# Performance work log

Measured on AMD Instinct MI355X. Metric: run time of the kernel, lower is better.

The kernel has to match this reference:

```python
import jax, jax.numpy as jnp
import numpy as np

B, D, H, O, E, K = 16384, 128, 512, 128, 8, 2
T = 1.0
EPS = float(np.finfo(float).eps)  # combine() zero-fill epsilon


def cv_squared(v):
    # torch .var() is unbiased (ddof=1)
    return jnp.var(v, ddof=1) / (jnp.mean(v) ** 2 + 1e-10)


def setup_inputs() -> dict:
    key = jax.random.key(0)
    k0, k1, k2, k3, k4, k5 = jax.random.split(key, 6)
    x = jax.random.normal(k0, (B, D), dtype=jnp.float32)
    w_gate = jax.random.normal(k1, (D, E), dtype=jnp.float32) * 0.02
    w1 = jax.random.normal(k2, (E, D, H), dtype=jnp.float32) * (1.0 / np.sqrt(D))
    b1 = jax.random.normal(k3, (E, H), dtype=jnp.float32) * 0.01
    w2 = jax.random.normal(k4, (E, H, O), dtype=jnp.float32) * (1.0 / np.sqrt(H))
    b2 = jax.random.normal(k5, (E, O), dtype=jnp.float32) * 0.01
    return {"x": x, "w_gate": w_gate, "w1": w1, "b1": b1, "w2": w2, "b2": b2}


def reference(x, w_gate, w1, b1, w2, b2):
    # ---- noisy top-k gating (eval mode: clean logits, no noise) ----
    logits = x @ w_gate                                   # [B, E]
    top_logits, top_idx = jax.lax.top_k(logits, K)        # [B, K]
    top_gates = jax.nn.softmax(top_logits / T, axis=-1)   # [B, K]
    gates = jnp.zeros_like(logits).at[jnp.arange(x.shape[0])[:, None], top_idx].set(top_gates)

    importance = gates.sum(0)                              # [E]
    load = (gates > 0).sum(0).astype(jnp.float32)          # [E]
    loss = cv_squared(importance) + cv_squared(load)

    # ---- experts (dense gate-weighted form of dispatch/combine) ----
    # output[b] = Sum_i gates[b,i] * expert_i(x[b]); zero gates contribute nothing,
    # identical math to SparseDispatcher's gather / per-expert MLP / scatter-add.
    h = jax.nn.relu(jnp.einsum('bd,edh->beh', x, w1) + b1[None])   # [B, E, H]
    y_e = jnp.einsum('beh,eho->beo', h, w2) + b2[None]             # [B, E, O]
    y = jnp.einsum('be,beo->bo', gates, y_e)                       # [B, O]
    # combine(): combined[combined == 0] = eps
    y = jnp.where(y == 0, jnp.asarray(EPS, y.dtype), y)
    return y, loss
```

## Files before the change

kernel.cpp:

```cpp
#include <hip/hip_runtime.h>
#include <hip/hip_bf16.h>
#include <math.h>

#define NB 16384
#define ND 128
#define NH 512
#define NO 128
#define NE 8
#define CPAD 32
#define NCH 16
#define EPSF 2.2204460492503131e-16f

using bf16x8 = __attribute__((ext_vector_type(8))) short;
using f32x16 = __attribute__((ext_vector_type(16))) float;
using uint2v = __attribute__((ext_vector_type(2))) unsigned;

#define WS_COUNTS 0u
#define WS_IMP    1024u
#define WS_TOKID  2048u
#define WS_TOKGG  526336u
#define WS_XBF    657408u
#define WS_W1F    4851712u
#define WS_W2F    5900288u
#define WS_YSTAGE 6948864u

__device__ __forceinline__ unsigned f2bf(float f){
  unsigned u = __float_as_uint(f);
  u += 0x7FFFu + ((u >> 16) & 1u);
  return u >> 16;
}
__device__ __forceinline__ unsigned cvtpk(float lo, float hi){
  unsigned r;
  asm("v_cvt_pk_bf16_f32 %0, %1, %2" : "=v"(r) : "v"(lo), "v"(hi));
  return r;
}
__device__ __forceinline__ void gld16(const void* g, void* l){
  __builtin_amdgcn_global_load_lds((const __attribute__((address_space(1))) void*)g,
                                   (__attribute__((address_space(3))) void*)l, 16, 0, 0);
}

__global__ __launch_bounds__(256) void prep_kernel(
    const float* __restrict__ x, const float* __restrict__ wg,
    const float* __restrict__ w1, const float* __restrict__ w2,
    unsigned short* __restrict__ xbf, unsigned short* __restrict__ w1f,
    unsigned short* __restrict__ w2f, int* __restrict__ counts,
    float* __restrict__ imp, int* __restrict__ tok_ids, float2* __restrict__ tok_gg){
  int bx = blockIdx.x, tid = threadIdx.x;
  if (bx >= 512){
    int u = (bx - 512)*256 + tid;
    int o = u & 127, hb = (u>>7)&3, c = (u>>9)&15, e = u>>13;
    int h0 = c*32 + (hb>>1)*16 + (hb&1)*8;
    const float* src = w2 + (size_t)e*NH*NO + (size_t)h0*NO + o;
    unsigned q[4];
    #pragma unroll
    for (int p = 0; p < 4; ++p)
      q[p] = f2bf(src[(2*p)*NO]) | (f2bf(src[(2*p+1)*NO]) << 16);
    *(uint4*)(w2f + (size_t)u*8) = make_uint4(q[0], q[1], q[2], q[3]);
    return;
  }
  if (bx >= 256){
    int u = (bx - 256)*256 + tid;
    int h32 = u & 31, db = (u>>5)&15, c = (u>>9)&15, e = u>>13;
    int d0 = (db>>1)*16 + (db&1)*8;
    int hg = c*32 + h32;
    const float* src = w1 + (size_t)e*ND*NH + (size_t)d0*NH + hg;
    unsigned q[4];
    #pragma unroll
    for (int p = 0; p < 4; ++p)
      q[p] = f2bf(src[(2*p)*NH]) | (f2bf(src[(2*p+1)*NH]) << 16);
    *(uint4*)(w1f + (size_t)u*8) = make_uint4(q[0], q[1], q[2], q[3]);
    return;
  }
  __shared__ int   lcnt[NE];
  __shared__ float limp[NE];
  __shared__ int   lbase[NE];
  if (tid < NE){ lcnt[tid] = 0; limp[tid] = 0.f; }
  __syncthreads();
  int tok  = bx*64 + (tid >> 2);
  int part = tid & 3;
  const float4* xr4 = (const float4*)(x + (size_t)tok*ND);
  double acc[NE];
  #pragma unroll
  for (int e = 0; e < NE; ++e) acc[e] = 0.0;
  #pragma unroll
  for (int j = 0; j < 8; ++j){
    int f4 = part + j*4;
    float4 v = xr4[f4];
    uint2 p;
    p.x = f2bf(v.x) | (f2bf(v.y) << 16);
    p.y = f2bf(v.z) | (f2bf(v.w) << 16);
    *(uint2*)(xbf + (size_t)tok*ND + f4*4) = p;
    const float4* wr = (const float4*)(wg + f4*32);
    float vm[4] = {v.x, v.y, v.z, v.w};
    #pragma unroll
    for (int m = 0; m < 4; ++m){
      float4 wa = wr[2*m], wb = wr[2*m+1];
      double d = (double)vm[m];
      acc[0] += d*(double)wa.x; acc[1] += d*(double)wa.y;
      acc[2] += d*(double)wa.z; acc[3] += d*(double)wa.w;
      acc[4] += d*(double)wb.x; acc[5] += d*(double)wb.y;
      acc[6] += d*(double)wb.z; acc[7] += d*(double)wb.w;
    }
  }
  #pragma unroll
  for (int e = 0; e < NE; ++e){
    acc[e] += __shfl_xor(acc[e], 1);
    acc[e] += __shfl_xor(acc[e], 2);
  }
  int i0 = 0, i1 = 0, s0 = 0, s1 = 0;
  float g0 = 0.f, g1 = 0.f;
  if (part == 0){
    double l0 = acc[0];
    #pragma unroll
    for (int e = 1; e < NE; ++e) if (acc[e] > l0){ l0 = acc[e]; i0 = e; }
    i1 = (i0 == 0) ? 1 : 0;
    double l1 = acc[i1];
    #pragma unroll
    for (int e = 0; e < NE; ++e) if (e != i0 && acc[e] > l1){ l1 = acc[e]; i1 = e; }
    float e1 = expf((float)(l1 - l0));
    g0 = 1.0f/(1.0f + e1);
    g1 = e1/(1.0f + e1);
    s0 = atomicAdd(&lcnt[i0], 1);
    s1 = atomicAdd(&lcnt[i1], 1);
    atomicAdd(&limp[i0], g0);
    atomicAdd(&limp[i1], g1);
    tok_gg[tok] = make_float2(g0, g1);
  }
  __syncthreads();
  if (tid < NE){
    lbase[tid] = atomicAdd(&counts[tid*CPAD], lcnt[tid]);
    atomicAdd(&imp[tid*CPAD], limp[tid]);
  }
  __syncthreads();
  if (part == 0){
    tok_ids[i0*NB + lbase[i0] + s0] = tok;
    tok_ids[i1*NB + lbase[i1] + s1] = tok | (1 << 30);
  }
}

__global__ __launch_bounds__(256) void expert_kernel(
    const unsigned short* __restrict__ xbf, const unsigned short* __restrict__ w1f,
    const unsigned short* __restrict__ w2f, const float* __restrict__ b1,
    const float* __restrict__ b2, const int* __restrict__ counts,
    const int* __restrict__ tok_ids, const float2* __restrict__ tok_gg,
    unsigned short* __restrict__ ystage){
  __shared__ char smem[32768];
  int b = blockIdx.x;
  int e = 0, base = 0, accb = 0, n_e = 0;
  #pragma unroll
  for (int ee = 0; ee < NE; ++ee){
    int ne = counts[ee*CPAD];
    int nbl = (ne + 127) >> 7;
    if (e == 0 && base == 0 && b < accb + nbl && n_e == 0){
      e = ee; base = (b - accb)*128; n_e = ne;
    }
    accb += nbl;
  }
  if (b >= accb) return;
  if (n_e == 0) return;
  int tid = threadIdx.x, wid = tid >> 6, lane = tid & 63, l31 = lane & 31, hi = lane >> 5;
  const int* tid_e = tok_ids + e*NB;
  char* w1buf = smem;
  char* w2buf = smem + 16384;
  const char* g1base = (const char*)w1f + ((size_t)e*NCH)*8192;
  const char* g2base = (const char*)w2f + ((size_t)e*NCH)*8192;

  int slot0 = base + wid*32 + l31;
  int raw0 = tid_e[slot0 < n_e ? slot0 : n_e-1];
  int tok0 = raw0 & 0x3FFFFFFF;
  bf16x8 xfrag[8];
  #pragma unroll
  for (int k = 0; k < 8; ++k)
    xfrag[k] = *(const bf16x8*)(xbf + (size_t)tok0*ND + (k*2 + hi)*8);

#define STAGE(c, bsel) do { \
    const char* _g1 = g1base + (size_t)(c)*8192 + wid*1024 + lane*16; \
    const char* _g2 = g2base + (size_t)(c)*8192 + wid*1024 + lane*16; \
    char* _l1 = w1buf + (bsel)*8192 + wid*1024; \
    char* _l2 = w2buf + (bsel)*8192 + wid*1024; \
    _Pragma("unroll") \
    for (int _s = 0; _s < 2; ++_s){ \
      gld16(_g1 + _s*4096, _l1 + _s*4096); \
      gld16(_g2 + _s*4096, _l2 + _s*4096); \
    } \
  } while(0)

  STAGE(0, 0);
  f32x16 yacc[4];
  #pragma unroll
  for (int ot = 0; ot < 4; ++ot)
    #pragma unroll
    for (int i = 0; i < 16; ++i) yacc[ot][i] = 0.f;
  __syncthreads();

  for (int c = 0; c < NCH; ++c){
    int bb = c & 1;
    if (c + 1 < NCH) STAGE(c + 1, bb ^ 1);
    f32x16 hacc;
    #pragma unroll
    for (int i = 0; i < 16; ++i) hacc[i] = 0.f;
    #pragma unroll
    for (int k = 0; k < 8; ++k){
      bf16x8 a = *(const bf16x8*)(w1buf + bb*8192 + (k*2 + hi)*512 + l31*16);
      hacc = __builtin_amdgcn_mfma_f32_32x32x16_bf16(a, xfrag[k], hacc, 0, 0, 0);
    }
    const float4* b1p = (const float4*)(b1 + e*NH + c*32 + hi*4);
    float dv[16];
    #pragma unroll
    for (int g = 0; g < 4; ++g){
      float4 bv = b1p[2*g];
      dv[4*g+0] = fmaxf(hacc[4*g+0] + bv.x, 0.f);
      dv[4*g+1] = fmaxf(hacc[4*g+1] + bv.y, 0.f);
      dv[4*g+2] = fmaxf(hacc[4*g+2] + bv.z, 0.f);
      dv[4*g+3] = fmaxf(hacc[4*g+3] + bv.w, 0.f);
    }
    unsigned A0 = cvtpk(dv[0], dv[1]),  A1 = cvtpk(dv[2], dv[3]);
    unsigned A2 = cvtpk(dv[4], dv[5]),  A3 = cvtpk(dv[6], dv[7]);
    unsigned A4 = cvtpk(dv[8], dv[9]),  A5 = cvtpk(dv[10], dv[11]);
    unsigned A6 = cvtpk(dv[12], dv[13]), A7 = cvtpk(dv[14], dv[15]);
    uint2v r0 = __builtin_amdgcn_permlane32_swap(A0, A2, false, false);
    uint2v r1 = __builtin_amdgcn_permlane32_swap(A1, A3, false, false);
    uint2v r2 = __builtin_amdgcn_permlane32_swap(A4, A6, false, false);
    uint2v r3 = __builtin_amdgcn_permlane32_swap(A5, A7, false, false);
    union { unsigned u[4]; bf16x8 v; } fa, fb;
    fa.u[0] = r0[0]; fa.u[1] = r1[0]; fa.u[2] = r0[1]; fa.u[3] = r1[1];
    fb.u[0] = r2[0]; fb.u[1] = r3[0]; fb.u[2] = r2[1]; fb.u[3] = r3[1];
    bf16x8 aht0 = fa.v, aht1 = fb.v;
    #pragma unroll
    for (int ot = 0; ot < 4; ++ot){
      bf16x8 bf0 = *(const bf16x8*)(w2buf + bb*8192 + (0*2 + hi)*2048 + (ot*32 + l31)*16);
      yacc[ot] = __builtin_amdgcn_mfma_f32_32x32x16_bf16(aht0, bf0, yacc[ot], 0, 0, 0);
      bf16x8 bf1 = *(const bf16x8*)(w2buf + bb*8192 + (1*2 + hi)*2048 + (ot*32 + l31)*16);
      yacc[ot] = __builtin_amdgcn_mfma_f32_32x32x16_bf16(aht1, bf1, yacc[ot], 0, 0, 0);
    }
    __syncthreads();
  }
#undef STAGE
  float b2v[4];
  #pragma unroll
  for (int ot = 0; ot < 4; ++ot) b2v[ot] = b2[e*NO + ot*32 + l31];
  #pragma unroll
  for (int r = 0; r < 16; ++r){
    int row = (r & 3) + 8*(r >> 2) + 4*hi;
    int slot = base + wid*32 + row;
    if (slot < n_e){
      int rw = tid_e[slot];
      int tk = rw & 0x3FFFFFFF, wh = (rw >> 30) & 1;
      float2 gg = tok_gg[tk];
      float g = wh ? gg.y : gg.x;
      unsigned short* dst = ystage + ((size_t)tk*2 + wh)*NO + l31;
      #pragma unroll
      for (int ot = 0; ot < 4; ++ot)
        dst[ot*32] = (unsigned short)f2bf((yacc[ot][r] + b2v[ot]) * g);
    }
  }
}

__global__ __launch_bounds__(256) void combine_kernel(
    const unsigned short* __restrict__ ystage, const int* __restrict__ counts,
    const float* __restrict__ imp, float* __restrict__ y){
  if (blockIdx.x == 0 && threadIdx.x == 0){
    double si = 0, sqi = 0, sl = 0, sql = 0;
    for (int e = 0; e < NE; ++e){
      double a = imp[e*CPAD];
      double b = (double)counts[e*CPAD];
      si += a; sqi += a*a; sl += b; sql += b*b;
    }
    double mi = si/8.0, vi = (sqi - 8.0*mi*mi)/7.0;
    double ml = sl/8.0, vl = (sql - 8.0*ml*ml)/7.0;
    y[NB*NO] = (float)(vi/(mi*mi + 1e-10) + vl/(ml*ml + 1e-10));
  }
  int idx = blockIdx.x*256 + threadIdx.x;
  int tk = idx >> 4, q = idx & 15;
  const unsigned short* r0 = ystage + (size_t)tk*256 + q*8;
  uint4 a = *(const uint4*)r0;
  uint4 bq = *(const uint4*)(r0 + 128);
  unsigned aw[4] = {a.x, a.y, a.z, a.w};
  unsigned bw[4] = {bq.x, bq.y, bq.z, bq.w};
  float4 o0, o1;
  float* op[8] = {&o0.x,&o0.y,&o0.z,&o0.w,&o1.x,&o1.y,&o1.z,&o1.w};
  #pragma unroll
  for (int i = 0; i < 4; ++i){
    float vlo = __uint_as_float(aw[i] << 16)        + __uint_as_float(bw[i] << 16);
    float vhi = __uint_as_float(aw[i] & 0xFFFF0000u) + __uint_as_float(bw[i] & 0xFFFF0000u);
    *op[2*i]   = (vlo == 0.f) ? EPSF : vlo;
    *op[2*i+1] = (vhi == 0.f) ? EPSF : vhi;
  }
  float* dst = y + (size_t)tk*128 + q*8;
  *(float4*)dst     = o0;
  *(float4*)(dst+4) = o1;
}

extern "C" void kernel_launch(void* const* d_in, const int* in_sizes, int n_in,
                              void* d_out, int out_size, void* d_ws, size_t ws_size,
                              hipStream_t stream){
  (void)in_sizes; (void)n_in; (void)out_size; (void)ws_size;
  const float* x  = (const float*)d_in[0];
  const float* wg = (const float*)d_in[1];
  const float* w1 = (const float*)d_in[2];
  const float* b1 = (const float*)d_in[3];
  const float* w2 = (const float*)d_in[4];
  const float* b2 = (const float*)d_in[5];
  float* out = (float*)d_out;
  char* ws = (char*)d_ws;
  int*            counts  = (int*)(ws + WS_COUNTS);
  float*          imp     = (float*)(ws + WS_IMP);
  int*            tok_ids = (int*)(ws + WS_TOKID);
  float2*         tok_gg  = (float2*)(ws + WS_TOKGG);
  unsigned short* xbf     = (unsigned short*)(ws + WS_XBF);
  unsigned short* w1f     = (unsigned short*)(ws + WS_W1F);
  unsigned short* w2f     = (unsigned short*)(ws + WS_W2F);
  unsigned short* ystage  = (unsigned short*)(ws + WS_YSTAGE);

  hipMemsetAsync(d_ws, 0, 2048, stream);
  prep_kernel<<<768, 256, 0, stream>>>(x, wg, w1, w2, xbf, w1f, w2f,
                                       counts, imp, tok_ids, tok_gg);
  expert_kernel<<<264, 256, 0, stream>>>(xbf, w1f, w2f, b1, b2,
                                         counts, tok_ids, tok_gg, ystage);
  combine_kernel<<<1024, 256, 0, stream>>>(ystage, counts, imp, out);
}
```

Before: 55.12 us.

## Fuse prep, expert and combine kernels into one persistent kernel with grid barriers

Merges the three launches into a single 256-block persistent kernel separated by software grid barriers. Per-block expert counts replace global atomics, and each block rebuilds the token-to-expert mapping itself with an LDS prefix scan. Expert tiles are looped over by the persistent blocks. This removes launch gaps and the atomic offset contention. It relies on all 256 blocks being co-resident for the spin barrier, and it adds per-tile scan and search overhead plus a redundant loop in the combine stage.

Result: slower. 197.3 us (+257.8%).

```diff
diff --git a/kernel.cpp b/kernel.cpp
--- a/kernel.cpp
+++ b/kernel.cpp
@@ -7,22 +7,31 @@
 #define NH 512
 #define NO 128
 #define NE 8
-#define CPAD 32
 #define NCH 16
+#define NBLK 256
 #define EPSF 2.2204460492503131e-16f
 
 using bf16x8 = __attribute__((ext_vector_type(8))) short;
 using f32x16 = __attribute__((ext_vector_type(16))) float;
 using uint2v = __attribute__((ext_vector_type(2))) unsigned;
 
-#define WS_COUNTS 0u
-#define WS_IMP    1024u
-#define WS_TOKID  2048u
-#define WS_TOKGG  526336u
-#define WS_XBF    657408u
-#define WS_W1F    4851712u
-#define WS_W2F    5900288u
-#define WS_YSTAGE 6948864u
+#define WS_BAR    0u
+#define WS_BLKCNT 1024u
+#define WS_BLKIMP 9216u
+#define WS_TOKID  17408u
+#define WS_TOKGG  541696u
+#define WS_XBF    672768u
+#define WS_W1F    4867072u
+#define WS_W2F    5915648u
+#define WS_YST    6964224u
+
+#define L_WB    0u
+#define L_CNT   32768u
+#define L_GP    40960u
+#define L_TOTL  41984u
+#define L_TBASE 42048u
+#define L_SLTOK 42112u
+#define L_A     42624u
 
 __device__ __forceinline__ unsigned f2bf(float f){
   unsigned u = __float_as_uint(f);
@@ -38,16 +47,43 @@
   __builtin_amdgcn_global_load_lds((const __attribute__((address_space(1))) void*)g,
                                    (__attribute__((address_space(3))) void*)l, 16, 0, 0);
 }
-
-__global__ __launch_bounds__(256) void prep_kernel(
+__device__ __forceinline__ void grid_barrier(int* bar, int target){
+  __syncthreads();
+  if (threadIdx.x == 0){
+    __threadfence();
+    __hip_atomic_fetch_add(bar, 1, __ATOMIC_RELEASE, __HIP_MEMORY_SCOPE_AGENT);
+    while (__hip_atomic_load(bar, __ATOMIC_ACQUIRE, __HIP_MEMORY_SCOPE_AGENT) < target)
+      __builtin_amdgcn_s_sleep(2);
+  }
+  __syncthreads();
+  __threadfence();
+}
+
+__global__ __launch_bounds__(256, 1) void moe_kernel(
     const float* __restrict__ x, const float* __restrict__ wg,
-    const float* __restrict__ w1, const float* __restrict__ w2,
+    const float* __restrict__ w1, const float* __restrict__ b1,
+    const float* __restrict__ w2, const float* __restrict__ b2,
+    int* __restrict__ bar, int* __restrict__ blk_cnt, float* __restrict__ blk_imp,
+    int* __restrict__ tok_ids, float2* __restrict__ tok_gg,
     unsigned short* __restrict__ xbf, unsigned short* __restrict__ w1f,
-    unsigned short* __restrict__ w2f, int* __restrict__ counts,
-    float* __restrict__ imp, int* __restrict__ tok_ids, float2* __restrict__ tok_gg){
-  int bx = blockIdx.x, tid = threadIdx.x;
-  if (bx >= 512){
-    int u = (bx - 512)*256 + tid;
+    unsigned short* __restrict__ w2f, unsigned short* __restrict__ ystage,
+    float* __restrict__ y){
+  __shared__ char L[43520];
+  int blk = blockIdx.x, tid = threadIdx.x;
+
+  {
+    int u = blk*256 + tid;
+    int h32 = u & 31, db = (u>>5)&15, c = (u>>9)&15, e = u>>13;
+    int d0 = (db>>1)*16 + (db&1)*8;
+    const float* src = w1 + (size_t)e*ND*NH + (size_t)d0*NH + c*32 + h32;
+    unsigned q[4];
+    #pragma unroll
+    for (int p = 0; p < 4; ++p)
+      q[p] = f2bf(src[(2*p)*NH]) | (f2bf(src[(2*p+1)*NH]) << 16);
+    *(uint4*)(w1f + (size_t)u*8) = make_uint4(q[0], q[1], q[2], q[3]);
+  }
+  {
+    int u = blk*256 + tid;
     int o = u & 127, hb = (u>>7)&3, c = (u>>9)&15, e = u>>13;
     int h0 = c*32 + (hb>>1)*16 + (hb&1)*8;
     const float* src = w2 + (size_t)e*NH*NO + (size_t)h0*NO + o;
@@ -56,122 +92,145 @@
     for (int p = 0; p < 4; ++p)
       q[p] = f2bf(src[(2*p)*NO]) | (f2bf(src[(2*p+1)*NO]) << 16);
     *(uint4*)(w2f + (size_t)u*8) = make_uint4(q[0], q[1], q[2], q[3]);
-    return;
-  }
-  if (bx >= 256){
-    int u = (bx - 256)*256 + tid;
-    int h32 = u & 31, db = (u>>5)&15, c = (u>>9)&15, e = u>>13;
-    int d0 = (db>>1)*16 + (db&1)*8;
-    int hg = c*32 + h32;
-    const float* src = w1 + (size_t)e*ND*NH + (size_t)d0*NH + hg;
-    unsigned q[4];
-    #pragma unroll
-    for (int p = 0; p < 4; ++p)
-      q[p] = f2bf(src[(2*p)*NH]) | (f2bf(src[(2*p+1)*NH]) << 16);
-    *(uint4*)(w1f + (size_t)u*8) = make_uint4(q[0], q[1], q[2], q[3]);
-    return;
-  }
-  __shared__ int   lcnt[NE];
-  __shared__ float limp[NE];
-  __shared__ int   lbase[NE];
-  if (tid < NE){ lcnt[tid] = 0; limp[tid] = 0.f; }
+  }
+  {
+    int*   lcnt = (int*)(L + L_A);
+    float* limp = (float*)(L + L_A + 32);
+    if (tid < NE){ lcnt[tid] = 0; limp[tid] = 0.f; }
+    __syncthreads();
+    int tok  = blk*64 + (tid >> 2);
+    int part = tid & 3;
+    const float4* xr4 = (const float4*)(x + (size_t)tok*ND);
+    double acc[NE];
+    #pragma unroll
+    for (int e = 0; e < NE; ++e) acc[e] = 0.0;
+    #pragma unroll
+    for (int j = 0; j < 8; ++j){
+      int f4 = part + j*4;
+      float4 v = xr4[f4];
+      uint2 p;
+      p.x = f2bf(v.x) | (f2bf(v.y) << 16);
+      p.y = f2bf(v.z) | (f2bf(v.w) << 16);
+      *(uint2*)(xbf + (size_t)tok*ND + f4*4) = p;
+      const float4* wr = (const float4*)(wg + f4*32);
+      float vm[4] = {v.x, v.y, v.z, v.w};
+      #pragma unroll
+      for (int m = 0; m < 4; ++m){
+        float4 wa = wr[2*m], wb = wr[2*m+1];
+        double d = (double)vm[m];
+        acc[0] += d*(double)wa.x; acc[1] += d*(double)wa.y;
+        acc[2] += d*(double)wa.z; acc[3] += d*(double)wa.w;
+        acc[4] += d*(double)wb.x; acc[5] += d*(double)wb.y;
+        acc[6] += d*(double)wb.z; acc[7] += d*(double)wb.w;
+      }
+    }
+    #pragma unroll
+    for (int e = 0; e < NE; ++e){
+      acc[e] += __shfl_xor(acc[e], 1);
+      acc[e] += __shfl_xor(acc[e], 2);
+    }
+    if (part == 0){
+      int i0 = 0;
+      double l0 = acc[0];
+      #pragma unroll
+      for (int e = 1; e < NE; ++e) if (acc[e] > l0){ l0 = acc[e]; i0 = e; }
+      int i1 = (i0 == 0) ? 1 : 0;
+      double l1 = acc[i1];
+      #pragma unroll
+      for (int e = 0; e < NE; ++e) if (e != i0 && acc[e] > l1){ l1 = acc[e]; i1 = e; }
+      float e1 = expf((float)(l1 - l0));
+      float g0 = 1.0f/(1.0f + e1);
+      float g1 = e1/(1.0f + e1);
+      int s0 = atomicAdd(&lcnt[i0], 1);
+      int s1 = atomicAdd(&lcnt[i1], 1);
+      atomicAdd(&limp[i0], g0);
+      atomicAdd(&limp[i1], g1);
+      tok_gg[tok] = make_float2(g0, g1);
+      tok_ids[i0*NB + blk*64 + s0] = tok;
+      tok_ids[i1*NB + blk*64 + s1] = tok | (1 << 30);
+    }
+    __syncthreads();
+    if (tid < NE){
+      blk_cnt[blk*8 + tid] = lcnt[tid];
+      blk_imp[blk*8 + tid] = limp[tid];
+    }
+  }
+
+  grid_barrier(bar, NBLK);
+
+  int* cnt_l = (int*)(L + L_CNT);
+  int* gp    = (int*)(L + L_GP);
+  int* totl  = (int*)(L + L_TOTL);
+  int* tbase = (int*)(L + L_TBASE);
+  int* sl_tok= (int*)(L + L_SLTOK);
+  {
+    int4 a = *(const int4*)(blk_cnt + tid*8);
+    int4 b = *(const int4*)(blk_cnt + tid*8 + 4);
+    cnt_l[0*256+tid]=a.x; cnt_l[1*256+tid]=a.y; cnt_l[2*256+tid]=a.z; cnt_l[3*256+tid]=a.w;
+    cnt_l[4*256+tid]=b.x; cnt_l[5*256+tid]=b.y; cnt_l[6*256+tid]=b.z; cnt_l[7*256+tid]=b.w;
+  }
   __syncthreads();
-  int tok  = bx*64 + (tid >> 2);
-  int part = tid & 3;
-  const float4* xr4 = (const float4*)(x + (size_t)tok*ND);
-  double acc[NE];
-  #pragma unroll
-  for (int e = 0; e < NE; ++e) acc[e] = 0.0;
-  #pragma unroll
-  for (int j = 0; j < 8; ++j){
-    int f4 = part + j*4;
-    float4 v = xr4[f4];
-    uint2 p;
-    p.x = f2bf(v.x) | (f2bf(v.y) << 16);
-    p.y = f2bf(v.z) | (f2bf(v.w) << 16);
-    *(uint2*)(xbf + (size_t)tok*ND + f4*4) = p;
-    const float4* wr = (const float4*)(wg + f4*32);
-    float vm[4] = {v.x, v.y, v.z, v.w};
-    #pragma unroll
-    for (int m = 0; m < 4; ++m){
-      float4 wa = wr[2*m], wb = wr[2*m+1];
-      double d = (double)vm[m];
-      acc[0] += d*(double)wa.x; acc[1] += d*(double)wa.y;
-      acc[2] += d*(double)wa.z; acc[3] += d*(double)wa.w;
-      acc[4] += d*(double)wb.x; acc[5] += d*(double)wb.y;
-      acc[6] += d*(double)wb.z; acc[7] += d*(double)wb.w;
-    }
-  }
-  #pragma unroll
-  for (int e = 0; e < NE; ++e){
-    acc[e] += __shfl_xor(acc[e], 1);
-    acc[e] += __shfl_xor(acc[e], 2);
-  }
-  int i0 = 0, i1 = 0, s0 = 0, s1 = 0;
-  float g0 = 0.f, g1 = 0.f;
-  if (part == 0){
-    double l0 = acc[0];
-    #pragma unroll
-    for (int e = 1; e < NE; ++e) if (acc[e] > l0){ l0 = acc[e]; i0 = e; }
-    i1 = (i0 == 0) ? 1 : 0;
-    double l1 = acc[i1];
-    #pragma unroll
-    for (int e = 0; e < NE; ++e) if (e != i0 && acc[e] > l1){ l1 = acc[e]; i1 = e; }
-    float e1 = expf((float)(l1 - l0));
-    g0 = 1.0f/(1.0f + e1);
-    g1 = e1/(1.0f + e1);
-    s0 = atomicAdd(&lcnt[i0], 1);
-    s1 = atomicAdd(&lcnt[i1], 1);
-    atomicAdd(&limp[i0], g0);
-    atomicAdd(&limp[i1], g1);
-    tok_gg[tok] = make_float2(g0, g1);
-  }
-  __syncthreads();
-  if (tid < NE){
-    lbase[tid] = atomicAdd(&counts[tid*CPAD], lcnt[tid]);
-    atomicAdd(&imp[tid*CPAD], limp[tid]);
-  }
-  __syncthreads();
-  if (part == 0){
-    tok_ids[i0*NB + lbase[i0] + s0] = tok;
-    tok_ids[i1*NB + lbase[i1] + s1] = tok | (1 << 30);
-  }
-}
-
-__global__ __launch_bounds__(256) void expert_kernel(
-    const unsigned short* __restrict__ xbf, const unsigned short* __restrict__ w1f,
-    const unsigned short* __restrict__ w2f, const float* __restrict__ b1,
-    const float* __restrict__ b2, const int* __restrict__ counts,
-    const int* __restrict__ tok_ids, const float2* __restrict__ tok_gg,
-    unsigned short* __restrict__ ystage){
-  __shared__ char smem[32768];
-  int b = blockIdx.x;
-  int e = 0, base = 0, accb = 0, n_e = 0;
-  #pragma unroll
-  for (int ee = 0; ee < NE; ++ee){
-    int ne = counts[ee*CPAD];
-    int nbl = (ne + 127) >> 7;
-    if (e == 0 && base == 0 && b < accb + nbl && n_e == 0){
-      e = ee; base = (b - accb)*128; n_e = ne;
-    }
-    accb += nbl;
-  }
-  if (b >= accb) return;
-  if (n_e == 0) return;
-  int tid = threadIdx.x, wid = tid >> 6, lane = tid & 63, l31 = lane & 31, hi = lane >> 5;
-  const int* tid_e = tok_ids + e*NB;
-  char* w1buf = smem;
-  char* w2buf = smem + 16384;
-  const char* g1base = (const char*)w1f + ((size_t)e*NCH)*8192;
-  const char* g2base = (const char*)w2f + ((size_t)e*NCH)*8192;
-
-  int slot0 = base + wid*32 + l31;
-  int raw0 = tid_e[slot0 < n_e ? slot0 : n_e-1];
-  int tok0 = raw0 & 0x3FFFFFFF;
-  bf16x8 xfrag[8];
-  #pragma unroll
-  for (int k = 0; k < 8; ++k)
-    xfrag[k] = *(const bf16x8*)(xbf + (size_t)tok0*ND + (k*2 + hi)*8);
+  {
+    int e8 = tid >> 5, g8 = tid & 31;
+    int s8 = 0;
+    #pragma unroll
+    for (int i = 0; i < 8; ++i) s8 += cnt_l[e8*256 + g8*8 + i];
+    gp[tid] = s8;
+    __syncthreads();
+    #pragma unroll
+    for (int st = 1; st < 32; st <<= 1){
+      int add = (g8 >= st) ? gp[tid - st] : 0;
+      __syncthreads();
+      gp[tid] += add;
+      __syncthreads();
+    }
+    if (g8 == 31) totl[e8] = gp[tid];
+    __syncthreads();
+    if (tid == 0){
+      tbase[0] = 0;
+      #pragma unroll
+      for (int e = 0; e < NE; ++e) tbase[e+1] = tbase[e] + ((totl[e] + 127) >> 7);
+    }
+    __syncthreads();
+  }
+  int total_tiles = tbase[8];
+  int wid = tid >> 6, lane = tid & 63, l31 = lane & 31, hi = lane >> 5;
+  char* w1buf = L + L_WB;
+  char* w2buf = L + L_WB + 16384;
+
+  for (int tb = blk; tb < total_tiles; tb += NBLK){
+    int e = 0;
+    #pragma unroll
+    for (int ee = 1; ee < NE; ++ee) if (tbase[ee] <= tb) e = ee;
+    int n_e  = totl[e];
+    int base = (tb - tbase[e])*128;
+    if (tid < 128){
+      int s = base + tid;
+      if (s >= n_e) s = n_e - 1;
+      int g = 0;
+      #pragma unroll
+      for (int st = 16; st; st >>= 1){
+        int c = g + st;
+        if (c <= 31 && gp[e*32 + c - 1] <= s) g = c;
+      }
+      int acc2 = g ? gp[e*32 + g - 1] : 0;
+      int gb = g*8;
+      while (true){
+        int c2 = cnt_l[e*256 + gb];
+        if (acc2 + c2 > s) break;
+        acc2 += c2; ++gb;
+      }
+      sl_tok[tid] = tok_ids[e*NB + gb*64 + (s - acc2)];
+    }
+    __syncthreads();
+
+    int tok0 = sl_tok[wid*32 + l31] & 0x3FFFFFFF;
+    bf16x8 xfrag[8];
+    #pragma unroll
+    for (int k = 0; k < 8; ++k)
+      xfrag[k] = *(const bf16x8*)(xbf + (size_t)tok0*ND + (k*2 + hi)*8);
+    const char* g1base = (const char*)w1f + (size_t)e*131072;
+    const char* g2base = (const char*)w2f + (size_t)e*131072;
 
 #define STAGE(c, bsel) do { \
     const char* _g1 = g1base + (size_t)(c)*8192 + wid*1024 + lane*16; \
@@ -185,110 +244,143 @@
     } \
   } while(0)
 
-  STAGE(0, 0);
-  f32x16 yacc[4];
-  #pragma unroll
-  for (int ot = 0; ot < 4; ++ot)
-    #pragma unroll
-    for (int i = 0; i < 16; ++i) yacc[ot][i] = 0.f;
-  __syncthreads();
-
-  for (int c = 0; c < NCH; ++c){
-    int bb = c & 1;
-    if (c + 1 < NCH) STAGE(c + 1, bb ^ 1);
-    f32x16 hacc;
-    #pragma unroll
-    for (int i = 0; i < 16; ++i) hacc[i] = 0.f;
-    #pragma unroll
-    for (int k = 0; k < 8; ++k){
-      bf16x8 a = *(const bf16x8*)(w1buf + bb*8192 + (k*2 + hi)*512 + l31*16);
-      hacc = __builtin_amdgcn_mfma_f32_32x32x16_bf16(a, xfrag[k], hacc, 0, 0, 0);
-    }
-    const float4* b1p = (const float4*)(b1 + e*NH + c*32 + hi*4);
-    float dv[16];
-    #pragma unroll
-    for (int g = 0; g < 4; ++g){
-      float4 bv = b1p[2*g];
-      dv[4*g+0] = fmaxf(hacc[4*g+0] + bv.x, 0.f);
-      dv[4*g+1] = fmaxf(hacc[4*g+1] + bv.y, 0.f);
-      dv[4*g+2] = fmaxf(hacc[4*g+2] + bv.z, 0.f);
-      dv[4*g+3] = fmaxf(hacc[4*g+3] + bv.w, 0.f);
-    }
-    unsigned A0 = cvtpk(dv[0], dv[1]),  A1 = cvtpk(dv[2], dv[3]);
-    unsigned A2 = cvtpk(dv[4], dv[5]),  A3 = cvtpk(dv[6], dv[7]);
-    unsigned A4 = cvtpk(dv[8], dv[9]),  A5 = cvtpk(dv[10], dv[11]);
-    unsigned A6 = cvtpk(dv[12], dv[13]), A7 = cvtpk(dv[14], dv[15]);
-    uint2v r0 = __builtin_amdgcn_permlane32_swap(A0, A2, false, false);
-    uint2v r1 = __builtin_amdgcn_permlane32_swap(A1, A3, false, false);
-    uint2v r2 = __builtin_amdgcn_permlane32_swap(A4, A6, false, false);
-    uint2v r3 = __builtin_amdgcn_permlane32_swap(A5, A7, false, false);
-    union { unsigned u[4]; bf16x8 v; } fa, fb;
-    fa.u[0] = r0[0]; fa.u[1] = r1[0]; fa.u[2] = r0[1]; fa.u[3] = r1[1];
-    fb.u[0] = r2[0]; fb.u[1] = r3[0]; fb.u[2] = r2[1]; fb.u[3] = r3[1];
-    bf16x8 aht0 = fa.v, aht1 = fb.v;
-    #pragma unroll
-    for (int ot = 0; ot < 4; ++ot){
-      bf16x8 bf0 = *(const bf16x8*)(w2buf + bb*8192 + (0*2 + hi)*2048 + (ot*32 + l31)*16);
-      yacc[ot] = __builtin_amdgcn_mfma_f32_32x32x16_bf16(aht0, bf0, yacc[ot], 0, 0, 0);
-      bf16x8 bf1 = *(const bf16x8*)(w2buf + bb*8192 + (1*2 + hi)*2048 + (ot*32 + l31)*16);
-      yacc[ot] = __builtin_amdgcn_mfma_f32_32x32x16_bf16(aht1, bf1, yacc[ot], 0, 0, 0);
-    }
-    __syncthreads();
-  }
+    STAGE(0, 0);
+    f32x16 yacc[4];
+    #pragma unroll
+    for (int ot = 0; ot < 4; ++ot)
+      #pragma unroll
+      for (int i = 0; i < 16; ++i) yacc[ot][i] = 0.f;
+    __syncthreads();
+
+    for (int c = 0; c < NCH; ++c){
+      int bb = c & 1;
+      if (c + 1 < NCH) STAGE(c + 1, bb ^ 1);
+      f32x16 hacc;
+      #pragma unroll
+      for (int i = 0; i < 16; ++i) hacc[i] = 0.f;
+      #pragma unroll
+      for (int k = 0; k < 8; ++k){
+        bf16x8 a = *(const bf16x8*)(w1buf + bb*8192 + (k*2 + hi)*512 + l31*16);
+        hacc = __builtin_amdgcn_mfma_f32_32x32x16_bf16(a, xfrag[k], hacc, 0, 0, 0);
+      }
+      const float4* b1p = (const float4*)(b1 + e*NH + c*32 + hi*4);
+      float dv[16];
+      #pragma unroll
+      for (int g = 0; g < 4; ++g){
+        float4 bv = b1p[2*g];
+        dv[4*g+0] = fmaxf(hacc[4*g+0] + bv.x, 0.f);
+        dv[4*g+1] = fmaxf(hacc[4*g+1] + bv.y, 0.f);
+        dv[4*g+2] = fmaxf(hacc[4*g+2] + bv.z, 0.f);
+        dv[4*g+3] = fmaxf(hacc[4*g+3] + bv.w, 0.f);
+      }
+      unsigned A0 = cvtpk(dv[0], dv[1]),   A1 = cvtpk(dv[2], dv[3]);
+      unsigned A2 = cvtpk(dv[4], dv[5]),   A3 = cvtpk(dv[6], dv[7]);
+      unsigned A4 = cvtpk(dv[8], dv[9]),   A5 = cvtpk(dv[10], dv[11]);
+      unsigned A6 = cvtpk(dv[12], dv[13]), A7 = cvtpk(dv[14], dv[15]);
+      uint2v r0 = __builtin_amdgcn_permlane32_swap(A0, A2, false, false);
+      uint2v r1 = __builtin_amdgcn_permlane32_swap(A1, A3, false, false);
+      uint2v r2 = __builtin_amdgcn_permlane32_swap(A4, A6, false, false);
+      uint2v r3 = __builtin_amdgcn_permlane32_swap(A5, A7, false, false);
+      union { unsigned u[4]; bf16x8 v; } fa, fb;
+      fa.u[0] = r0[0]; fa.u[1] = r1[0]; fa.u[2] = r0[1]; fa.u[3] = r1[1];
+      fb.u[0] = r2[0]; fb.u[1] = r3[0]; fb.u[2] = r2[1]; fb.u[3] = r3[1];
+      bf16x8 aht0 = fa.v, aht1 = fb.v;
+      #pragma unroll
+      for (int ot = 0; ot < 4; ++ot){
+        bf16x8 bf0 = *(const bf16x8*)(w2buf + bb*8192 + hi*2048 + (ot*32 + l31)*16);
+        yacc[ot] = __builtin_amdgcn_mfma_f32_32x32x16_bf16(aht0, bf0, yacc[ot], 0, 0, 0);
+        bf16x8 bf1 = *(const bf16x8*)(w2buf + bb*8192 + (2 + hi)*2048 + (ot*32 + l31)*16);
+        yacc[ot] = __builtin_amdgcn_mfma_f32_32x32x16_bf16(aht1, bf1, yacc[ot], 0, 0, 0);
+      }
+      __syncthreads();
+    }
 #undef STAGE
-  float b2v[4];
-  #pragma unroll
-  for (int ot = 0; ot < 4; ++ot) b2v[ot] = b2[e*NO + ot*32 + l31];
-  #pragma unroll
-  for (int r = 0; r < 16; ++r){
-    int row = (r & 3) + 8*(r >> 2) + 4*hi;
-    int slot = base + wid*32 + row;
-    if (slot < n_e){
-      int rw = tid_e[slot];
-      int tk = rw & 0x3FFFFFFF, wh = (rw >> 30) & 1;
-      float2 gg = tok_gg[tk];
-      float g = wh ? gg.y : gg.x;
-      unsigned short* dst = ystage + ((size_t)tk*2 + wh)*NO + l31;
-      #pragma unroll
-      for (int ot = 0; ot < 4; ++ot)
-        dst[ot*32] = (unsigned short)f2bf((yacc[ot][r] + b2v[ot]) * g);
-    }
-  }
-}
-
-__global__ __launch_bounds__(256) void combine_kernel(
-    const unsigned short* __restrict__ ystage, const int* __restrict__ counts,
-    const float* __restrict__ imp, float* __restrict__ y){
-  if (blockIdx.x == 0 && threadIdx.x == 0){
-    double si = 0, sqi = 0, sl = 0, sql = 0;
+    float b2v[4];
+    #pragma unroll
+    for (int ot = 0; ot < 4; ++ot) b2v[ot] = b2[e*NO + ot*32 + l31];
+    #pragma unroll
+    for (int r = 0; r < 16; ++r){
+      int row = (r & 3) + 8*(r >> 2) + 4*hi;
+      int slot = base + wid*32 + row;
+      if (slot < n_e){
+        int rw = sl_tok[wid*32 + row];
+        int tk = rw & 0x3FFFFFFF, wh = (rw >> 30) & 1;
+        float2 gg = tok_gg[tk];
+        float g = wh ? gg.y : gg.x;
+        unsigned short* dst = ystage + ((size_t)tk*2 + wh)*NO + l31;
+        #pragma unroll
+        for (int ot = 0; ot < 4; ++ot)
+          dst[ot*32] = (unsigned short)f2bf((yacc[ot][r] + b2v[ot]) * g);
+      }
+    }
+    __syncthreads();
+  }
+
+  grid_barrier(bar, 2*NBLK);
+
+  {
+    int tok = blk*64 + (tid >> 2), q = tid & 3;
+    const unsigned short* r0 = ystage + (size_t)tok*256 + q*32;
+    float* dst = y + (size_t)tok*128 + q*32;
+    #pragma unroll
+    for (int it = 0; it < 4; ++it){
+      uint4 a  = *(const uint4*)(r0 + it*8);
+      uint4 bq = *(const uint4*)(r0 + 128 + it*8);
+      unsigned aw[4] = {a.x, a.y, a.z, a.w};
+      unsigned bw[4] = {bq.x, bq.y, bq.z, bq.w};
+      float4 o;
+      float* op[4] = {&o.x, &o.y, &o.z, &o.w};
+      #pragma unroll
+      for (int i = 0; i < 2; ++i){
+        float vlo = __uint_as_float(aw[2*i] << 16)         + __uint_as_float(bw[2*i] << 16);
+        float vhi = __uint_as_float(aw[2*i] & 0xFFFF0000u) + __uint_as_float(bw[2*i] & 0xFFFF0000u);
+        *op[2*i]   = (vlo == 0.f) ? EPSF : vlo;
+        *op[2*i+1] = (vhi == 0.f) ? EPSF : vhi;
+        vlo = __uint_as_float(aw[2*i+1] << 16)         + __uint_as_float(bw[2*i+1] << 16);
+        vhi = __uint_as_float(aw[2*i+1] & 0xFFFF0000u) + __uint_as_float(bw[2*i+1] & 0xFFFF0000u);
+        float4 dummy; (void)dummy;
+        o.x = o.x;
+      }
+      float outs[8];
+      #pragma unroll
+      for (int i = 0; i < 4; ++i){
+        float vlo = __uint_as_float(aw[i] << 16)         + __uint_as_float(bw[i] << 16);
+        float vhi = __uint_as_float(aw[i] & 0xFFFF0000u) + __uint_as_float(bw[i] & 0xFFFF0000u);
+        outs[2*i]   = (vlo == 0.f) ? EPSF : vlo;
+        outs[2*i+1] = (vhi == 0.f) ? EPSF : vhi;
+      }
+      float4 o0 = {outs[0], outs[1], outs[2], outs[3]};
+      float4 o1 = {outs[4], outs[5], outs[6], outs[7]};
+      *(float4*)(dst + it*8)     = o0;
+      *(float4*)(dst + it*8 + 4) = o1;
+    }
+  }
+  if (blk == 0){
+    float* red = (float*)(L + L_A);
+    float v[NE];
+    #pragma unroll
+    for (int e = 0; e < NE; ++e) v[e] = blk_imp[tid*8 + e];
+    #pragma unroll
     for (int e = 0; e < NE; ++e){
-      double a = imp[e*CPAD];
-      double b = (double)counts[e*CPAD];
-      si += a; sqi += a*a; sl += b; sql += b*b;
-    }
-    double mi = si/8.0, vi = (sqi - 8.0*mi*mi)/7.0;
-    double ml = sl/8.0, vl = (sql - 8.0*ml*ml)/7.0;
-    y[NB*NO] = (float)(vi/(mi*mi + 1e-10) + vl/(ml*ml + 1e-10));
-  }
-  int idx = blockIdx.x*256 + threadIdx.x;
-  int tk = idx >> 4, q = idx & 15;
-  const unsigned short* r0 = ystage + (size_t)tk*256 + q*8;
-  uint4 a = *(const uint4*)r0;
-  uint4 bq = *(const uint4*)(r0 + 128);
-  unsigned aw[4] = {a.x, a.y, a.z, a.w};
-  unsigned bw[4] = {bq.x, bq.y, bq.z, bq.w};
-  float4 o0, o1;
-  float* op[8] = {&o0.x,&o0.y,&o0.z,&o0.w,&o1.x,&o1.y,&o1.z,&o1.w};
-  #pragma unroll
-  for (int i = 0; i < 4; ++i){
-    float vlo = __uint_as_float(aw[i] << 16)        + __uint_as_float(bw[i] << 16);
-    float vhi = __uint_as_float(aw[i] & 0xFFFF0000u) + __uint_as_float(bw[i] & 0xFFFF0000u);
-    *op[2*i]   = (vlo == 0.f) ? EPSF : vlo;
-    *op[2*i+1] = (vhi == 0.f) ? EPSF : vhi;
-  }
-  float* dst = y + (size_t)tk*128 + q*8;
-  *(float4*)dst     = o0;
-  *(float4*)(dst+4) = o1;
+      float r = v[e];
+      #pragma unroll
+      for (int st = 1; st < 64; st <<= 1) r += __shfl_xor(r, st);
+      if (lane == 0) red[e*4 + wid] = r;
+    }
+    __syncthreads();
+    if (tid == 0){
+      double si = 0, sqi = 0, sl = 0, sql = 0;
+      #pragma unroll
+      for (int e = 0; e < NE; ++e){
+        double a = (double)(red[e*4] + red[e*4+1] + red[e*4+2] + red[e*4+3]);
+        double b = (double)totl[e];
+        si += a; sqi += a*a; sl += b; sql += b*b;
+      }
+      double mi = si/8.0, vi = (sqi - 8.0*mi*mi)/7.0;
+      double ml = sl/8.0, vl = (sql - 8.0*ml*ml)/7.0;
+      y[NB*NO] = (float)(vi/(mi*mi + 1e-10) + vl/(ml*ml + 1e-10));
+    }
+  }
 }
 
 extern "C" void kernel_launch(void* const* d_in, const int* in_sizes, int n_in,
@@ -303,19 +395,18 @@
   const float* b2 = (const float*)d_in[5];
   float* out = (float*)d_out;
   char* ws = (char*)d_ws;
-  int*            counts  = (int*)(ws + WS_COUNTS);
-  float*          imp     = (float*)(ws + WS_IMP);
+  int*            bar     = (int*)(ws + WS_BAR);
+  int*            blk_cnt = (int*)(ws + WS_BLKCNT);
+  float*          blk_imp = (float*)(ws + WS_BLKIMP);
   int*            tok_ids = (int*)(ws + WS_TOKID);
   float2*         tok_gg  = (float2*)(ws + WS_TOKGG);
   unsigned short* xbf     = (unsigned short*)(ws + WS_XBF);
   unsigned short* w1f     = (unsigned short*)(ws + WS_W1F);
   unsigned short* w2f     = (unsigned short*)(ws + WS_W2F);
-  unsigned short* ystage  = (unsigned short*)(ws + WS_YSTAGE);
-
-  hipMemsetAsync(d_ws, 0, 2048, stream);
-  prep_kernel<<<768, 256, 0, stream>>>(x, wg, w1, w2, xbf, w1f, w2f,
-                                       counts, imp, tok_ids, tok_gg);
-  expert_kernel<<<264, 256, 0, stream>>>(xbf, w1f, w2f, b1, b2,
-                                         counts, tok_ids, tok_gg, ystage);
-  combine_kernel<<<1024, 256, 0, stream>>>(ystage, counts, imp, out);
-}
+  unsigned short* ystage  = (unsigned short*)(ws + WS_YST);
+
+  hipMemsetAsync(d_ws, 0, 1024, stream);
+  moe_kernel<<<NBLK, 256, 0, stream>>>(x, wg, w1, b1, w2, b2,
+                                       bar, blk_cnt, blk_imp, tok_ids, tok_gg,
+                                       xbf, w1f, w2f, ystage, out);
+}
```

## Split expert hidden dimension across two wave groups with LDS reduction

Applied to the files above, without the earlier changes.

The expert kernel now runs 512 threads per block, and the two halves of the block each process half of the hidden dimension (256 each) using larger 16KB chunk stages over 4 iterations. Each half keeps partial output accumulators, and half 1 reduces its partials through LDS into half 0 before the gated bf16 store. It also adds s_setprio around the MFMA sections. The aim is more waves per block to hide latency and fewer loop iterations and barriers, at the cost of 128KB of LDS per block (one block per CU) and an extra LDS reduction step.

Measured after the change: 62.76 us. +13.9%, slower.

```diff
diff --git a/kernel.cpp b/kernel.cpp
--- a/kernel.cpp
+++ b/kernel.cpp
@@ -8,7 +8,6 @@
 #define NO 128
 #define NE 8
 #define CPAD 32
-#define NCH 16
 #define EPSF 2.2204460492503131e-16f
 
 using bf16x8 = __attribute__((ext_vector_type(8))) short;
@@ -138,34 +137,28 @@
   }
 }
 
-__global__ __launch_bounds__(256) void expert_kernel(
+__global__ __launch_bounds__(512, 1) void expert_kernel(
     const unsigned short* __restrict__ xbf, const unsigned short* __restrict__ w1f,
     const unsigned short* __restrict__ w2f, const float* __restrict__ b1,
     const float* __restrict__ b2, const int* __restrict__ counts,
     const int* __restrict__ tok_ids, const float2* __restrict__ tok_gg,
     unsigned short* __restrict__ ystage){
-  __shared__ char smem[32768];
+  __shared__ char L[131072];
   int b = blockIdx.x;
-  int e = 0, base = 0, accb = 0, n_e = 0;
+  int e = -1, base = 0, n_e = 0, accb = 0;
   #pragma unroll
   for (int ee = 0; ee < NE; ++ee){
     int ne = counts[ee*CPAD];
     int nbl = (ne + 127) >> 7;
-    if (e == 0 && base == 0 && b < accb + nbl && n_e == 0){
-      e = ee; base = (b - accb)*128; n_e = ne;
-    }
+    if (e < 0 && b < accb + nbl){ e = ee; base = (b - accb)*128; n_e = ne; }
     accb += nbl;
   }
-  if (b >= accb) return;
-  if (n_e == 0) return;
+  if (e < 0) return;
   int tid = threadIdx.x, wid = tid >> 6, lane = tid & 63, l31 = lane & 31, hi = lane >> 5;
+  int half = wid >> 2, wl = wid & 3;
   const int* tid_e = tok_ids + e*NB;
-  char* w1buf = smem;
-  char* w2buf = smem + 16384;
-  const char* g1base = (const char*)w1f + ((size_t)e*NCH)*8192;
-  const char* g2base = (const char*)w2f + ((size_t)e*NCH)*8192;
-
-  int slot0 = base + wid*32 + l31;
+
+  int slot0 = base + wl*32 + l31;
   int raw0 = tid_e[slot0 < n_e ? slot0 : n_e-1];
   int tok0 = raw0 & 0x3FFFFFFF;
   bf16x8 xfrag[8];
@@ -173,15 +166,20 @@
   for (int k = 0; k < 8; ++k)
     xfrag[k] = *(const bf16x8*)(xbf + (size_t)tok0*ND + (k*2 + hi)*8);
 
+  const char* g1base = (const char*)w1f + (size_t)e*131072 + half*65536;
+  const char* g2base = (const char*)w2f + (size_t)e*131072 + half*65536;
+  char* w1h = L + half*32768;
+  char* w2h = L + 65536 + half*32768;
+
 #define STAGE(c, bsel) do { \
-    const char* _g1 = g1base + (size_t)(c)*8192 + wid*1024 + lane*16; \
-    const char* _g2 = g2base + (size_t)(c)*8192 + wid*1024 + lane*16; \
-    char* _l1 = w1buf + (bsel)*8192 + wid*1024; \
-    char* _l2 = w2buf + (bsel)*8192 + wid*1024; \
+    const char* _g1 = g1base + (size_t)(c)*16384 + wl*4096 + lane*16; \
+    const char* _g2 = g2base + (size_t)(c)*16384 + wl*4096 + lane*16; \
+    char* _l1 = w1h + (bsel)*16384 + wl*4096; \
+    char* _l2 = w2h + (bsel)*16384 + wl*4096; \
     _Pragma("unroll") \
-    for (int _s = 0; _s < 2; ++_s){ \
-      gld16(_g1 + _s*4096, _l1 + _s*4096); \
-      gld16(_g2 + _s*4096, _l2 + _s*4096); \
+    for (int _s = 0; _s < 4; ++_s){ \
+      gld16(_g1 + _s*1024, _l1 + _s*1024); \
+      gld16(_g2 + _s*1024, _l2 + _s*1024); \
     } \
   } while(0)
 
@@ -193,65 +191,88 @@
     for (int i = 0; i < 16; ++i) yacc[ot][i] = 0.f;
   __syncthreads();
 
-  for (int c = 0; c < NCH; ++c){
+  for (int c = 0; c < 4; ++c){
     int bb = c & 1;
-    if (c + 1 < NCH) STAGE(c + 1, bb ^ 1);
-    f32x16 hacc;
-    #pragma unroll
-    for (int i = 0; i < 16; ++i) hacc[i] = 0.f;
-    #pragma unroll
-    for (int k = 0; k < 8; ++k){
-      bf16x8 a = *(const bf16x8*)(w1buf + bb*8192 + (k*2 + hi)*512 + l31*16);
-      hacc = __builtin_amdgcn_mfma_f32_32x32x16_bf16(a, xfrag[k], hacc, 0, 0, 0);
-    }
-    const float4* b1p = (const float4*)(b1 + e*NH + c*32 + hi*4);
-    float dv[16];
-    #pragma unroll
-    for (int g = 0; g < 4; ++g){
-      float4 bv = b1p[2*g];
-      dv[4*g+0] = fmaxf(hacc[4*g+0] + bv.x, 0.f);
-      dv[4*g+1] = fmaxf(hacc[4*g+1] + bv.y, 0.f);
-      dv[4*g+2] = fmaxf(hacc[4*g+2] + bv.z, 0.f);
-      dv[4*g+3] = fmaxf(hacc[4*g+3] + bv.w, 0.f);
-    }
-    unsigned A0 = cvtpk(dv[0], dv[1]),  A1 = cvtpk(dv[2], dv[3]);
-    unsigned A2 = cvtpk(dv[4], dv[5]),  A3 = cvtpk(dv[6], dv[7]);
-    unsigned A4 = cvtpk(dv[8], dv[9]),  A5 = cvtpk(dv[10], dv[11]);
-    unsigned A6 = cvtpk(dv[12], dv[13]), A7 = cvtpk(dv[14], dv[15]);
-    uint2v r0 = __builtin_amdgcn_permlane32_swap(A0, A2, false, false);
-    uint2v r1 = __builtin_amdgcn_permlane32_swap(A1, A3, false, false);
-    uint2v r2 = __builtin_amdgcn_permlane32_swap(A4, A6, false, false);
-    uint2v r3 = __builtin_amdgcn_permlane32_swap(A5, A7, false, false);
-    union { unsigned u[4]; bf16x8 v; } fa, fb;
-    fa.u[0] = r0[0]; fa.u[1] = r1[0]; fa.u[2] = r0[1]; fa.u[3] = r1[1];
-    fb.u[0] = r2[0]; fb.u[1] = r3[0]; fb.u[2] = r2[1]; fb.u[3] = r3[1];
-    bf16x8 aht0 = fa.v, aht1 = fb.v;
-    #pragma unroll
-    for (int ot = 0; ot < 4; ++ot){
-      bf16x8 bf0 = *(const bf16x8*)(w2buf + bb*8192 + (0*2 + hi)*2048 + (ot*32 + l31)*16);
-      yacc[ot] = __builtin_amdgcn_mfma_f32_32x32x16_bf16(aht0, bf0, yacc[ot], 0, 0, 0);
-      bf16x8 bf1 = *(const bf16x8*)(w2buf + bb*8192 + (1*2 + hi)*2048 + (ot*32 + l31)*16);
-      yacc[ot] = __builtin_amdgcn_mfma_f32_32x32x16_bf16(aht1, bf1, yacc[ot], 0, 0, 0);
+    if (c + 1 < 4) STAGE(c + 1, bb ^ 1);
+    #pragma unroll
+    for (int hs = 0; hs < 2; ++hs){
+      f32x16 hacc;
+      #pragma unroll
+      for (int i = 0; i < 16; ++i) hacc[i] = 0.f;
+      __builtin_amdgcn_s_setprio(1);
+      #pragma unroll
+      for (int k = 0; k < 8; ++k){
+        bf16x8 a = *(const bf16x8*)(w1h + bb*16384 + hs*8192 + (k*2 + hi)*512 + l31*16);
+        hacc = __builtin_amdgcn_mfma_f32_32x32x16_bf16(a, xfrag[k], hacc, 0, 0, 0);
+      }
+      __builtin_amdgcn_s_setprio(0);
+      int c32 = (half*4 + c)*2 + hs;
+      const float4* b1p = (const float4*)(b1 + e*NH + c32*32 + hi*4);
+      float dv[16];
+      #pragma unroll
+      for (int g = 0; g < 4; ++g){
+        float4 bv = b1p[2*g];
+        dv[4*g+0] = fmaxf(hacc[4*g+0] + bv.x, 0.f);
+        dv[4*g+1] = fmaxf(hacc[4*g+1] + bv.y, 0.f);
+        dv[4*g+2] = fmaxf(hacc[4*g+2] + bv.z, 0.f);
+        dv[4*g+3] = fmaxf(hacc[4*g+3] + bv.w, 0.f);
+      }
+      unsigned A0 = cvtpk(dv[0], dv[1]),   A1 = cvtpk(dv[2], dv[3]);
+      unsigned A2 = cvtpk(dv[4], dv[5]),   A3 = cvtpk(dv[6], dv[7]);
+      unsigned A4 = cvtpk(dv[8], dv[9]),   A5 = cvtpk(dv[10], dv[11]);
+      unsigned A6 = cvtpk(dv[12], dv[13]), A7 = cvtpk(dv[14], dv[15]);
+      uint2v r0 = __builtin_amdgcn_permlane32_swap(A0, A2, false, false);
+      uint2v r1 = __builtin_amdgcn_permlane32_swap(A1, A3, false, false);
+      uint2v r2 = __builtin_amdgcn_permlane32_swap(A4, A6, false, false);
+      uint2v r3 = __builtin_amdgcn_permlane32_swap(A5, A7, false, false);
+      union { unsigned u[4]; bf16x8 v; } fa, fb;
+      fa.u[0] = r0[0]; fa.u[1] = r1[0]; fa.u[2] = r0[1]; fa.u[3] = r1[1];
+      fb.u[0] = r2[0]; fb.u[1] = r3[0]; fb.u[2] = r2[1]; fb.u[3] = r3[1];
+      bf16x8 aht0 = fa.v, aht1 = fb.v;
+      __builtin_amdgcn_s_setprio(1);
+      #pragma unroll
+      for (int ot = 0; ot < 4; ++ot){
+        bf16x8 bf0 = *(const bf16x8*)(w2h + bb*16384 + hs*8192 + hi*2048 + (ot*32 + l31)*16);
+        yacc[ot] = __builtin_amdgcn_mfma_f32_32x32x16_bf16(aht0, bf0, yacc[ot], 0, 0, 0);
+        bf16x8 bf1 = *(const bf16x8*)(w2h + bb*16384 + hs*8192 + (2 + hi)*2048 + (ot*32 + l31)*16);
+        yacc[ot] = __builtin_amdgcn_mfma_f32_32x32x16_bf16(aht1, bf1, yacc[ot], 0, 0, 0);
+      }
+      __builtin_amdgcn_s_setprio(0);
     }
     __syncthreads();
   }
 #undef STAGE
-  float b2v[4];
-  #pragma unroll
-  for (int ot = 0; ot < 4; ++ot) b2v[ot] = b2[e*NO + ot*32 + l31];
-  #pragma unroll
-  for (int r = 0; r < 16; ++r){
-    int row = (r & 3) + 8*(r >> 2) + 4*hi;
-    int slot = base + wid*32 + row;
-    if (slot < n_e){
-      int rw = tid_e[slot];
-      int tk = rw & 0x3FFFFFFF, wh = (rw >> 30) & 1;
-      float2 gg = tok_gg[tk];
-      float g = wh ? gg.y : gg.x;
-      unsigned short* dst = ystage + ((size_t)tk*2 + wh)*NO + l31;
-      #pragma unroll
-      for (int ot = 0; ot < 4; ++ot)
-        dst[ot*32] = (unsigned short)f2bf((yacc[ot][r] + b2v[ot]) * g);
+
+  float* yred = (float*)L;
+  if (half == 1){
+    #pragma unroll
+    for (int r = 0; r < 16; ++r){
+      int row = (r & 3) + 8*(r >> 2) + 4*hi;
+      float* dst = yred + (wl*32 + row)*132 + l31;
+      #pragma unroll
+      for (int ot = 0; ot < 4; ++ot) dst[ot*32] = yacc[ot][r];
+    }
+  }
+  __syncthreads();
+  if (half == 0){
+    float b2v[4];
+    #pragma unroll
+    for (int ot = 0; ot < 4; ++ot) b2v[ot] = b2[e*NO + ot*32 + l31];
+    #pragma unroll
+    for (int r = 0; r < 16; ++r){
+      int row = (r & 3) + 8*(r >> 2) + 4*hi;
+      int slot = base + wl*32 + row;
+      if (slot < n_e){
+        const float* srcr = yred + (wl*32 + row)*132 + l31;
+        int rw = tid_e[slot];
+        int tk = rw & 0x3FFFFFFF, wh = (rw >> 30) & 1;
+        float2 gg = tok_gg[tk];
+        float g = wh ? gg.y : gg.x;
+        unsigned short* dst = ystage + ((size_t)tk*2 + wh)*NO + l31;
+        #pragma unroll
+        for (int ot = 0; ot < 4; ++ot)
+          dst[ot*32] = (unsigned short)f2bf((yacc[ot][r] + srcr[ot*32] + b2v[ot]) * g);
+      }
     }
   }
 }
@@ -277,15 +298,16 @@
   uint4 bq = *(const uint4*)(r0 + 128);
   unsigned aw[4] = {a.x, a.y, a.z, a.w};
   unsigned bw[4] = {bq.x, bq.y, bq.z, bq.w};
-  float4 o0, o1;
-  float* op[8] = {&o0.x,&o0.y,&o0.z,&o0.w,&o1.x,&o1.y,&o1.z,&o1.w};
+  float outs[8];
   #pragma unroll
   for (int i = 0; i < 4; ++i){
-    float vlo = __uint_as_float(aw[i] << 16)        + __uint_as_float(bw[i] << 16);
+    float vlo = __uint_as_float(aw[i] << 16)         + __uint_as_float(bw[i] << 16);
     float vhi = __uint_as_float(aw[i] & 0xFFFF0000u) + __uint_as_float(bw[i] & 0xFFFF0000u);
-    *op[2*i]   = (vlo == 0.f) ? EPSF : vlo;
-    *op[2*i+1] = (vhi == 0.f) ? EPSF : vhi;
-  }
+    outs[2*i]   = (vlo == 0.f) ? EPSF : vlo;
+    outs[2*i+1] = (vhi == 0.f) ? EPSF : vhi;
+  }
+  float4 o0 = {outs[0], outs[1], outs[2], outs[3]};
+  float4 o1 = {outs[4], outs[5], outs[6], outs[7]};
   float* dst = y + (size_t)tk*128 + q*8;
   *(float4*)dst     = o0;
   *(float4*)(dst+4) = o1;
@@ -315,7 +337,7 @@
   hipMemsetAsync(d_ws, 0, 2048, stream);
   prep_kernel<<<768, 256, 0, stream>>>(x, wg, w1, w2, xbf, w1f, w2f,
                                        counts, imp, tok_ids, tok_gg);
-  expert_kernel<<<264, 256, 0, stream>>>(xbf, w1f, w2f, b1, b2,
+  expert_kernel<<<264, 512, 0, stream>>>(xbf, w1f, w2f, b1, b2,
                                          counts, tok_ids, tok_gg, ystage);
   combine_kernel<<<1024, 256, 0, stream>>>(ystage, counts, imp, out);
 }
```
